# Optimization experiments

Hardware: AMD Instinct MI355X
Metric: run time of the kernel (lower is better)

## Reference

```python
import jax, jax.numpy as jnp
import numpy as np

EPS = 1e-5

def conv1x1(x, W, b):
    # x: (B,C,H,W), W: (O,C), b: (O,)
    return jnp.einsum('bchw,oc->bohw', x, W) + b[None, :, None, None]

def setup_inputs() -> dict:
    key = jax.random.key(0)
    ks = jax.random.split(key, 16)
    B, C_in, C1, D, K, H, Wd = 8, 512, 256, 128, 32, 96, 96
    s = lambda k, shape, fan: jax.random.normal(k, shape, jnp.float32) * (1.0 / np.sqrt(fan))
    return {
        'X': jax.random.normal(ks[0], (B, C_in, H, Wd), jnp.float32),
        'W_theta': s(ks[1], (C1, C_in), C_in), 'b_theta': jnp.zeros((C1,), jnp.float32),
        'W_phi': s(ks[2], (C1, C_in), C_in), 'b_phi': jnp.zeros((C1,), jnp.float32),
        'W_g': s(ks[3], (C1, C_in), C_in), 'b_g': jnp.zeros((C1,), jnp.float32),
        'W2': s(ks[4], (C_in, C1), C1), 'b2': jnp.zeros((C_in,), jnp.float32),
        'W3': s(ks[5], (D, C_in), C_in), 'b3': jnp.zeros((D,), jnp.float32),
        'codewords': jax.random.normal(ks[6], (K, D), jnp.float32),
        'scale': -jax.random.uniform(ks[7], (K,), jnp.float32),  # Deep-TEN init: U(-1,0)
        'W_fc': s(ks[8], (C_in, D), D), 'b_fc': jnp.zeros((C_in,), jnp.float32),
    }

def reference(X, W_theta, b_theta, W_phi, b_phi, W_g, b_g, W2, b2, W3, b3,
              codewords, scale, W_fc, b_fc):
    B, C_in, H, Wd = X.shape
    C1 = W_theta.shape[0]
    D, K = W3.shape[0], codewords.shape[0]
    N = H * Wd
    # --- non-local (channel-attention) block ---
    theta = conv1x1(X, W_theta, b_theta).reshape(B, C1, N)          # (B,C1,N)
    phi = conv1x1(X, W_phi, b_phi).reshape(B, C1, N)                # (B,C1,N)
    g = conv1x1(X, W_g, b_g).reshape(B, C1, N)                      # (B,C1,N)
    f = jax.nn.softmax(jnp.einsum('bcn,bdn->bcd', theta, phi), axis=-1)  # (B,C1,C1)
    y = jnp.einsum('bcd,bdn->bcn', f, g).reshape(B, C1, H, Wd)
    z = conv1x1(y, W2, b2) + X                                      # (B,C_in,H,W)
    # --- Deep-TEN encoding ---
    z_ = conv1x1(z, W3, b3)                                         # (B,D,H,W)
    x = z_.reshape(B, D, N).transpose(0, 2, 1)                      # (B,N,D)
    # squared L2 distances to codewords without (B,N,K,D) residuals
    dist = (jnp.sum(x * x, -1, keepdims=True)
            - 2.0 * jnp.einsum('bnd,kd->bnk', x, codewords)
            + jnp.sum(codewords * codewords, -1))                   # (B,N,K)
    A = jax.nn.softmax(scale * dist, axis=-1)                       # (B,N,K)
    # E_k = sum_i A_ik (x_i - c_k)
    E = jnp.einsum('bnk,bnd->bkd', A, x) - A.sum(1)[..., None] * codewords  # (B,K,D)
    # --- training-mode batch norm over K channels (no affine) ---
    mean = E.mean(axis=(0, 2), keepdims=True)
    var = E.var(axis=(0, 2), keepdims=True)
    e = jax.nn.relu((E - mean) * jax.lax.rsqrt(var + EPS))
    Es = e.sum(axis=1)                                              # (B,D)
    gamma = jax.nn.sigmoid(Es @ W_fc.T + b_fc)                      # (B,C_in)
    return z * gamma[:, :, None, None]
```

## Files before the change

### kernel.cpp

```cpp
#include <hip/hip_runtime.h>


typedef unsigned short u16;

#define Bb 8
#define Cc 512
#define C1 256
#define Dd 128
#define Kk 32
#define Nn 9216

typedef __attribute__((ext_vector_type(8))) short short8v;
typedef __attribute__((ext_vector_type(4))) short short4v;
typedef __attribute__((ext_vector_type(4))) float f32x4;

__device__ __forceinline__ float b2f(u16 u) {
  union { unsigned int i; float f; } v; v.i = ((unsigned int)u) << 16; return v.f;
}
__device__ __forceinline__ u16 f2b(float f) {
  union { float f; unsigned int i; } v; v.f = f;
  unsigned int x = v.i;
  return (u16)((x + 0x7fffu + ((x >> 16) & 1u)) >> 16);
}

__device__ __forceinline__ float4 load4(const float* p) { return *(const float4*)p; }
__device__ __forceinline__ float4 load4(const u16* p) {
  ushort4 q = *(const ushort4*)p;
  return make_float4(b2f(q.x), b2f(q.y), b2f(q.z), b2f(q.w));
}
__device__ __forceinline__ void store4(float* p, float a, float b, float c, float d) {
  *(float4*)p = make_float4(a, b, c, d);
}

__device__ __forceinline__ float waveSum(float v) {
  #pragma unroll
  for (int o = 32; o > 0; o >>= 1) v += __shfl_xor(v, o);
  return v;
}
__device__ __forceinline__ float waveMax(float v) {
  #pragma unroll
  for (int o = 32; o > 0; o >>= 1) v = fmaxf(v, __shfl_xor(v, o));
  return v;
}
__device__ __forceinline__ float blockSum256(float v) {
  __shared__ float sm[4];
  v = waveSum(v);
  if ((threadIdx.x & 63) == 0) sm[threadIdx.x >> 6] = v;
  __syncthreads();
  float r = sm[0] + sm[1] + sm[2] + sm[3];
  __syncthreads();
  return r;
}
__device__ __forceinline__ float blockMax256(float v) {
  __shared__ float sm[4];
  v = waveMax(v);
  if ((threadIdx.x & 63) == 0) sm[threadIdx.x >> 6] = v;
  __syncthreads();
  float r = fmaxf(fmaxf(sm[0], sm[1]), fmaxf(sm[2], sm[3]));
  __syncthreads();
  return r;
}

__device__ __forceinline__ f32x4 mfma_bf16_16x16x32(short8v a, short8v b, f32x4 c) {
  asm("v_mfma_f32_16x16x32_bf16 %0, %1, %2, %0" : "+v"(c) : "v"(a), "v"(b));
  return c;
}

__device__ __forceinline__ int fsw(int r) { return (r ^ (r >> 2) ^ (r >> 4)) & 3; }

__device__ __forceinline__ void cvt2(float x0, float x1, unsigned int& h, unsigned int& l) {
  asm("v_cvt_pk_bf16_f32 %0, %1, %2" : "=v"(h) : "v"(x0), "v"(x1));
  union { unsigned int u; float f; } fa, fb;
  fa.u = h << 16; fb.u = h & 0xffff0000u;
  float r0 = x0 - fa.f, r1 = x1 - fb.f;
  asm("v_cvt_pk_bf16_f32 %0, %1, %2" : "=v"(l) : "v"(r0), "v"(r1));
}

__device__ __forceinline__ void storeC4(float* p, float4 v) { *(float4*)p = v; }
__device__ __forceinline__ void storeC4(u16* p, float4 v) {
  ushort4 q; q.x = f2b(v.x); q.y = f2b(v.y); q.z = f2b(v.z); q.w = f2b(v.w);
  *(ushort4*)p = q;
}

template<typename TO, int OMODE, bool ADDI>
__global__ __launch_bounds__(256, 3) void gemm_mfma(
    const float* __restrict__ A, const float* __restrict__ B, TO* __restrict__ C,
    int N, int K,
    long long sA, long long sB, long long sC,
    const float* __restrict__ biasRow, long long sBias,
    int gnx, int gny)
{
  __shared__ __align__(16) u16 Asm_[2][128][40];
  __shared__ __align__(16) u16 Bsm_[2][128][40];

  int id = blockIdx.x;
  {
    const int nwg = gridDim.x;
    if ((nwg & 7) == 0) id = (id & 7) * (nwg >> 3) + (id >> 3);
  }
  const int per = gnx * gny;
  const int b = id / per;
  const int rem = id - b * per;
  const int by = rem % gny;
  const int bx = rem / gny;
  A += b * sA; B += b * sB; C += b * sC;
  const int m0 = by * 128, n0 = bx * 128;

  const int t = threadIdx.x;
  const int w = t >> 6, lane = t & 63;
  const int wr = w >> 1, wc = w & 1;
  const int lr = lane & 15, lq = lane >> 4;

  const int sar = t >> 1, sak = (t & 1) * 16;
  const int kg2 = t >> 4, ng = t & 15;

  float ra[16];
  float rb[16];

  auto loadA = [&](int k0) {
    const float* p = A + (long long)(m0 + sar) * K + (k0 + sak);
    #pragma unroll
    for (int i = 0; i < 4; ++i) {
      float4 v = *(const float4*)(p + i * 4);
      ra[i*4+0] = v.x; ra[i*4+1] = v.y; ra[i*4+2] = v.z; ra[i*4+3] = v.w;
    }
  };
  auto loadB = [&](int k0) {
    const float* p = B + (long long)(k0 + kg2 * 2) * N + (n0 + ng * 8);
    #pragma unroll
    for (int i = 0; i < 2; ++i) {
      float4 v0 = *(const float4*)(p + (long long)i * N);
      float4 v1 = *(const float4*)(p + (long long)i * N + 4);
      rb[i*8+0]=v0.x; rb[i*8+1]=v0.y; rb[i*8+2]=v0.z; rb[i*8+3]=v0.w;
      rb[i*8+4]=v1.x; rb[i*8+5]=v1.y; rb[i*8+6]=v1.z; rb[i*8+7]=v1.w;
    }
  };

  auto stage = [&]() {
    {
      const int f = fsw(sar);
      #pragma unroll
      for (int h = 0; h < 2; ++h) {
        const int col = ((((sak >> 3) + h) ^ f) << 3);
        union { unsigned int u[4]; short8v v; } H, L;
        #pragma unroll
        for (int p = 0; p < 4; ++p) cvt2(ra[h*8+2*p], ra[h*8+2*p+1], H.u[p], L.u[p]);
        *(short8v*)&Asm_[0][sar][col] = H.v;
        *(short8v*)&Asm_[1][sar][col] = L.v;
      }
    }
    {
      const int blk = kg2 >> 2, sub = 2 * (kg2 & 3);
      #pragma unroll
      for (int j = 0; j < 8; ++j) {
        const int n = ng * 8 + j;
        const int col = ((blk ^ fsw(n)) << 3) + sub;
        unsigned int H, L;
        cvt2(rb[j], rb[8 + j], H, L);
        *(unsigned int*)&Bsm_[0][n][col] = H;
        *(unsigned int*)&Bsm_[1][n][col] = L;
      }
    }
  };

  f32x4 acc[4][4];
  #pragma unroll
  for (int im = 0; im < 4; ++im)
    #pragma unroll
    for (int in = 0; in < 4; ++in)
      acc[im][in] = f32x4{0.f, 0.f, 0.f, 0.f};

  loadA(0); loadB(0);
  for (int k0 = 0; k0 < K; k0 += 32) {
    stage();
    if (k0 + 32 < K) { loadA(k0 + 32); loadB(k0 + 32); }
    __syncthreads();
    short8v af[2][4];
    #pragma unroll
    for (int im = 0; im < 4; ++im) {
      const int r = wr * 64 + im * 16 + lr;
      const int col = ((lq ^ fsw(r)) << 3);
      af[0][im] = *(const short8v*)&Asm_[0][r][col];
      af[1][im] = *(const short8v*)&Asm_[1][r][col];
    }
    #pragma unroll
    for (int in = 0; in < 4; ++in) {
      const int rB = wc * 64 + in * 16 + lr;
      const int colB = ((lq ^ fsw(rB)) << 3);
      short8v bh = *(const short8v*)&Bsm_[0][rB][colB];
      short8v bl = *(const short8v*)&Bsm_[1][rB][colB];
      #pragma unroll
      for (int im = 0; im < 4; ++im) {
        acc[im][in] = mfma_bf16_16x16x32(af[0][im], bh, acc[im][in]);
        acc[im][in] = mfma_bf16_16x16x32(af[0][im], bl, acc[im][in]);
        acc[im][in] = mfma_bf16_16x16x32(af[1][im], bh, acc[im][in]);
      }
    }
    __syncthreads();
  }
  asm volatile("s_nop 7\n\ts_nop 7\n\ts_nop 7");

  if constexpr (OMODE == 1) {
    const float* bb = biasRow + (long long)b * sBias;
    #pragma unroll
    for (int im = 0; im < 4; ++im) {
      #pragma unroll
      for (int in = 0; in < 4; ++in) {
        const f32x4 a = acc[im][in];
        const int gc = n0 + wc * 64 + in * 16 + lr;
        const int d0b = wr * 64 + im * 16 + lq * 4;
        float4 v = make_float4(a[0] + bb[d0b + 0], a[1] + bb[d0b + 1],
                               a[2] + bb[d0b + 2], a[3] + bb[d0b + 3]);
        storeC4(&C[(long long)gc * Dd + d0b], v);
      }
    }
  } else {
    #pragma unroll
    for (int im = 0; im < 4; ++im) {
      #pragma unroll
      for (int in = 0; in < 4; ++in) {
        const f32x4 a = acc[im][in];
        const int gc = n0 + wc * 64 + in * 16 + lr;
        #pragma unroll
        for (int p = 0; p < 4; ++p) {
          const int gr = m0 + wr * 64 + im * 16 + lq * 4 + p;
          float v = a[p];
          if (biasRow) v += biasRow[b * sBias + gr];
          if (ADDI && gr == gc) v += 1.f;
          C[(long long)gr * N + gc] = v;
        }
      }
    }
  }
}

__device__ __constant__ int PIa[10] = {0,0,0,0,1,1,1,2,2,3};
__device__ __constant__ int PJa[10] = {0,1,2,3,1,2,3,2,3,3};

__global__ __launch_bounds__(256, 3) void gxxt_kernel(
    const float* __restrict__ X, float* __restrict__ part,
    int numKS, int kChunk, float* __restrict__ sP)
{
  __shared__ __align__(16) u16 Asm_[2][128][40];
  __shared__ __align__(16) u16 Bsm_[2][64][40];

  int id = blockIdx.x;
  {
    const int nwg = gridDim.x;
    if ((nwg & 7) == 0) id = (id & 7) * (nwg >> 3) + (id >> 3);
  }
  const int sub = id % 20;
  const int pair = sub >> 1, jh = sub & 1;
  const int rest = id / 20;
  const int ks = rest % numKS;
  const int b = rest / numKS;
  const int i0 = PIa[pair] * 128, j0 = PJa[pair] * 128;
  const bool same = (i0 == j0);
  const bool doSum = same && (jh == 0);
  const float* Xb = X + (long long)b * Cc * Nn;
  const int kBeg = ks * kChunk, kEnd = kBeg + kChunk;

  const int t = threadIdx.x;
  const int w = t >> 6, lane = t & 63;
  const int wr = w >> 1, wc = w & 1;
  const int lr = lane & 15, lq = lane >> 4;
  const int sar = t >> 1, sak = (t & 1) * 16;
  const int sbr = t >> 2, sbk = (t & 3) * 8;

  float ra[16], rb[8];
  float rs = 0.f;

  auto loadA = [&](int k0) {
    const float* p = Xb + (long long)(i0 + sar) * Nn + (k0 + sak);
    #pragma unroll
    for (int i = 0; i < 4; ++i) {
      float4 v = *(const float4*)(p + i * 4);
      ra[i*4+0] = v.x; ra[i*4+1] = v.y; ra[i*4+2] = v.z; ra[i*4+3] = v.w;
    }
  };
  auto loadB = [&](int k0) {
    const float* p = Xb + (long long)(j0 + jh * 64 + sbr) * Nn + (k0 + sbk);
    float4 v0 = *(const float4*)(p);
    float4 v1 = *(const float4*)(p + 4);
    rb[0]=v0.x; rb[1]=v0.y; rb[2]=v0.z; rb[3]=v0.w;
    rb[4]=v1.x; rb[5]=v1.y; rb[6]=v1.z; rb[7]=v1.w;
  };
  auto stageA = [&]() {
    const int f = fsw(sar);
    #pragma unroll
    for (int h = 0; h < 2; ++h) {
      const int col = ((((sak >> 3) + h) ^ f) << 3);
      union { unsigned int u[4]; short8v v; } Hv, Lv;
      #pragma unroll
      for (int p = 0; p < 4; ++p) cvt2(ra[h*8+2*p], ra[h*8+2*p+1], Hv.u[p], Lv.u[p]);
      *(short8v*)&Asm_[0][sar][col] = Hv.v;
      *(short8v*)&Asm_[1][sar][col] = Lv.v;
    }
  };
  auto stageB = [&]() {
    const int col = (((sbk >> 3) ^ fsw(sbr)) << 3);
    union { unsigned int u[4]; short8v v; } Hv, Lv;
    #pragma unroll
    for (int p = 0; p < 4; ++p) cvt2(rb[2*p], rb[2*p+1], Hv.u[p], Lv.u[p]);
    *(short8v*)&Bsm_[0][sbr][col] = Hv.v;
    *(short8v*)&Bsm_[1][sbr][col] = Lv.v;
  };

  f32x4 acc[4][2];
  #pragma unroll
  for (int im = 0; im < 4; ++im)
    #pragma unroll
    for (int in = 0; in < 2; ++in)
      acc[im][in] = f32x4{0.f, 0.f, 0.f, 0.f};

  loadA(kBeg);
  if (!same) loadB(kBeg);
  for (int k0 = kBeg; k0 < kEnd; k0 += 32) {
    if (doSum) {
      #pragma unroll
      for (int j = 0; j < 16; ++j) rs += ra[j];
    }
    stageA();
    if (!same) stageB();
    if (k0 + 32 < kEnd) { loadA(k0 + 32); if (!same) loadB(k0 + 32); }
    __syncthreads();
    short8v af[2][4];
    #pragma unroll
    for (int im = 0; im < 4; ++im) {
      const int r = wr * 64 + im * 16 + lr;
      const int col = ((lq ^ fsw(r)) << 3);
      af[0][im] = *(const short8v*)&Asm_[0][r][col];
      af[1][im] = *(const short8v*)&Asm_[1][r][col];
    }
    #pragma unroll
    for (int in = 0; in < 2; ++in) {
      const int rloc = wc * 32 + in * 16 + lr;
      short8v bh, bl;
      if (same) {
        const int r = jh * 64 + rloc;
        const int colB = ((lq ^ fsw(r)) << 3);
        bh = *(const short8v*)&Asm_[0][r][colB];
        bl = *(const short8v*)&Asm_[1][r][colB];
      } else {
        const int colB = ((lq ^ fsw(rloc)) << 3);
        bh = *(const short8v*)&Bsm_[0][rloc][colB];
        bl = *(const short8v*)&Bsm_[1][rloc][colB];
      }
      #pragma unroll
      for (int im = 0; im < 4; ++im) {
        acc[im][in] = mfma_bf16_16x16x32(af[0][im], bh, acc[im][in]);
        acc[im][in] = mfma_bf16_16x16x32(af[0][im], bl, acc[im][in]);
        acc[im][in] = mfma_bf16_16x16x32(af[1][im], bh, acc[im][in]);
      }
    }
    __syncthreads();
  }
  asm volatile("s_nop 7\n\ts_nop 7\n\ts_nop 7");

  if (doSum) sP[((long long)ks * Bb + b) * Cc + i0 + sar] = rs;

  float* Cp = part + ((long long)(ks * Bb + b) * 10 + pair) * 16384 + jh * 64;
  #pragma unroll
  for (int im = 0; im < 4; ++im) {
    #pragma unroll
    for (int in = 0; in < 2; ++in) {
      const f32x4 a = acc[im][in];
      const int gc = wc * 32 + in * 16 + lr;
      #pragma unroll
      for (int p = 0; p < 4; ++p) {
        const int gr = wr * 64 + im * 16 + lq * 4 + p;
        Cp[gr * 128 + gc] = a[p];
      }
    }
  }
}

__global__ __launch_bounds__(256) void gred_kernel(const float* __restrict__ part,
    float* __restrict__ G, int numKS) {
  __shared__ float sm[64][129];
  const int pair = blockIdx.x % 10, b = blockIdx.x / 10;
  const int i0 = PIa[pair] * 128, j0 = PJa[pair] * 128;
  float* Gb = G + (long long)b * Cc * Cc;
  const long long ksStr = (long long)Bb * 10 * 16384;
  const float* p0 = part + ((long long)b * 10 + pair) * 16384;
  const int t = threadIdx.x;
  for (int half = 0; half < 2; ++half) {
    const int r0 = half * 64;
    __syncthreads();
    for (int rep = 0; rep < 32; ++rep) {
      int idx = r0 * 128 + rep * 256 + t;
      float s = 0.f;
      for (int ks = 0; ks < numKS; ++ks) s += p0[(long long)ks * ksStr + idx];
      int r = (idx >> 7) - r0, c = idx & 127;
      sm[r][c] = s;
      Gb[(long long)(i0 + r0 + r) * Cc + (j0 + c)] = s;
    }
    if (i0 != j0) {
      __syncthreads();
      for (int rep = 0; rep < 32; ++rep) {
        int o = rep * 256 + t;
        int rr = o >> 6, cc = o & 63;
        Gb[(long long)(j0 + rr) * Cc + (i0 + r0 + cc)] = sm[cc][rr];
      }
    }
  }
}

template<bool TRANSB>
__global__ __launch_bounds__(256) void gemm64(
    const float* __restrict__ A, const float* __restrict__ B, float* __restrict__ C,
    int M, int N, int K,
    long long sA, long long sB, long long sC,
    const float* __restrict__ biasRow, long long sBias)
{
  const int bz = blockIdx.z;
  A += (long long)bz * sA;
  B += (long long)bz * sB;
  C += (long long)bz * sC;
  const int m0 = blockIdx.y * 64, n0 = blockIdx.x * 64;
  __shared__ __align__(16) float As[16][64];
  __shared__ __align__(16) float Bs[16][64];
  const int t = threadIdx.x;
  const int lr = t >> 2, lk = (t & 3) << 2;
  const int tm = (t >> 4) << 2, tn = (t & 15) << 2;
  float acc[4][4] = {};
  for (int k0 = 0; k0 < K; k0 += 16) {
    {
      float4 a = load4(A + (long long)(m0 + lr) * K + (k0 + lk));
      As[lk + 0][lr] = a.x; As[lk + 1][lr] = a.y; As[lk + 2][lr] = a.z; As[lk + 3][lr] = a.w;
    }
    if (TRANSB) {
      float4 b = load4(B + (long long)(n0 + lr) * K + (k0 + lk));
      Bs[lk + 0][lr] = b.x; Bs[lk + 1][lr] = b.y; Bs[lk + 2][lr] = b.z; Bs[lk + 3][lr] = b.w;
    } else {
      const int kr = t >> 4, nc = (t & 15) << 2;
      float4 b = load4(B + (long long)(k0 + kr) * N + (n0 + nc));
      *(float4*)&Bs[kr][nc] = b;
    }
    __syncthreads();
    #pragma unroll
    for (int kk = 0; kk < 16; ++kk) {
      const float4 av = *(const float4*)&As[kk][tm];
      const float4 bv = *(const float4*)&Bs[kk][tn];
      acc[0][0] = fmaf(av.x, bv.x, acc[0][0]);
      acc[0][1] = fmaf(av.x, bv.y, acc[0][1]);
      acc[0][2] = fmaf(av.x, bv.z, acc[0][2]);
      acc[0][3] = fmaf(av.x, bv.w, acc[0][3]);
      acc[1][0] = fmaf(av.y, bv.x, acc[1][0]);
      acc[1][1] = fmaf(av.y, bv.y, acc[1][1]);
      acc[1][2] = fmaf(av.y, bv.z, acc[1][2]);
      acc[1][3] = fmaf(av.y, bv.w, acc[1][3]);
      acc[2][0] = fmaf(av.z, bv.x, acc[2][0]);
      acc[2][1] = fmaf(av.z, bv.y, acc[2][1]);
      acc[2][2] = fmaf(av.z, bv.z, acc[2][2]);
      acc[2][3] = fmaf(av.z, bv.w, acc[2][3]);
      acc[3][0] = fmaf(av.w, bv.x, acc[3][0]);
      acc[3][1] = fmaf(av.w, bv.y, acc[3][1]);
      acc[3][2] = fmaf(av.w, bv.z, acc[3][2]);
      acc[3][3] = fmaf(av.w, bv.w, acc[3][3]);
    }
    __syncthreads();
  }
  #pragma unroll
  for (int i = 0; i < 4; ++i) {
    const int m = m0 + tm + i;
    float bias = biasRow ? biasRow[bz * sBias + m] : 0.f;
    store4(C + (long long)m * N + (n0 + tn),
           acc[i][0] + bias, acc[i][1] + bias, acc[i][2] + bias, acc[i][3] + bias);
  }
}

__global__ __launch_bounds__(256) void gemv2_kernel(const float* __restrict__ Wth,
    const float* __restrict__ Wph, const float* __restrict__ sP, int numKS,
    float* __restrict__ u, float* __restrict__ v) {
  int b = blockIdx.x & 7, sel = blockIdx.x >> 3;
  const float* W = sel ? Wph : Wth;
  float* out = sel ? v : u;
  __shared__ float ssm[Cc];
  for (int i = threadIdx.x; i < Cc; i += 256) {
    float s = 0.f;
    for (int ks = 0; ks < numKS; ++ks) s += sP[((long long)ks * Bb + b) * Cc + i];
    ssm[i] = s;
  }
  __syncthreads();
  int i = threadIdx.x;
  const float* wr = W + i * Cc;
  float acc = 0.f;
  for (int k = 0; k < Cc; ++k) acc = fmaf(wr[k], ssm[k], acc);
  out[b * C1 + i] = acc;
}

__global__ __launch_bounds__(256) void softmax_kernel(float* __restrict__ L,
    const float* __restrict__ bth, const float* __restrict__ bph,
    const float* __restrict__ u, const float* __restrict__ v,
    const float* __restrict__ bg, float* __restrict__ w) {
  __shared__ float bgs[C1];
  int row = blockIdx.x;
  int b = row >> 8, i = row & 255;
  int j = threadIdx.x;
  bgs[j] = bg[j];
  float bt = bth[i], bp = bph[j];
  long long idx = (long long)row * C1 + j;
  float val = L[idx] + bt * v[b * C1 + j] + u[b * C1 + i] * bp + (float)Nn * bt * bp;
  float mx = blockMax256(val);
  float p = expf(val - mx);
  float sm = blockSum256(p);
  float f = p / sm;
  L[idx] = f;
  float ws = blockSum256(f * bgs[j]);
  if (j == 0) w[row] = ws;
}

__global__ __launch_bounds__(256) void q_kernel(const float* __restrict__ W2,
                                                const float* __restrict__ b2v,
                                                const float* __restrict__ w,
                                                float* __restrict__ q) {
  int gi = blockIdx.x * 256 + threadIdx.x;
  int b = gi >> 9, c = gi & 511;
  __shared__ float wsm[C1];
  wsm[threadIdx.x] = w[b * C1 + threadIdx.x];
  __syncthreads();
  const float* wr = W2 + c * C1;
  float acc = b2v[c];
  for (int i = 0; i < C1; ++i) acc = fmaf(wr[i], wsm[i], acc);
  q[gi] = acc;
}

__global__ __launch_bounds__(256) void zqbias_kernel(const float* __restrict__ W3,
    const float* __restrict__ b3, const float* __restrict__ q, float* __restrict__ zqb) {
  int gi = blockIdx.x * 256 + threadIdx.x;
  int b = gi >> 7, d = gi & 127;
  const float* wr = W3 + d * Cc;
  const float* qr = q + b * Cc;
  float acc = b3[d];
  for (int c = 0; c < Cc; ++c) acc = fmaf(wr[c], qr[c], acc);
  zqb[gi] = acc;
}

template<typename ZT>
__global__ __launch_bounds__(256) void enc_kernel(
    const ZT* __restrict__ zq,
    const float* __restrict__ cw,
    const float* __restrict__ sc,
    float* __restrict__ Eraw8,
    float* __restrict__ Asum8)
{
  __shared__ float csm[Kk][Dd + 1];
  __shared__ float cc[Kk], ssm[Kk];
  __shared__ float sA[Kk][256 + 1];
  __shared__ float zs[16][Dd + 4];
  const int tid = threadIdx.x;
  const int b = blockIdx.y;
  const int slot = blockIdx.x & 7;
  const int n0 = blockIdx.x * 256;

  #pragma unroll
  for (int r = 0; r < 16; ++r) {
    int idx = r * 256 + tid;
    csm[idx >> 7][idx & 127] = cw[idx];
  }
  if (tid < Kk) ssm[tid] = sc[tid];
  __syncthreads();
  if (tid < Kk) {
    float a = 0.f;
    for (int d = 0; d < Dd; ++d) { float cv = csm[tid][d]; a = fmaf(cv, cv, a); }
    cc[tid] = a;
  }
  __syncthreads();

  const ZT* zrow = zq + ((long long)b * Nn + n0 + tid) * Dd;
  float dots[Kk];
  #pragma unroll
  for (int k = 0; k < Kk; ++k) dots[k] = 0.f;
  float xx = 0.f;
  for (int d = 0; d < Dd; d += 4) {
    float4 xv = load4(zrow + d);
    xx = fmaf(xv.x, xv.x, xx); xx = fmaf(xv.y, xv.y, xx);
    xx = fmaf(xv.z, xv.z, xx); xx = fmaf(xv.w, xv.w, xx);
    #pragma unroll
    for (int k = 0; k < Kk; ++k) {
      float dk = dots[k];
      dk = fmaf(csm[k][d + 0], xv.x, dk);
      dk = fmaf(csm[k][d + 1], xv.y, dk);
      dk = fmaf(csm[k][d + 2], xv.z, dk);
      dk = fmaf(csm[k][d + 3], xv.w, dk);
      dots[k] = dk;
    }
  }
  float mx = -1e30f;
  #pragma unroll
  for (int k = 0; k < Kk; ++k) {
    float l = ssm[k] * (xx - 2.f * dots[k] + cc[k]);
    dots[k] = l;
    mx = fmaxf(mx, l);
  }
  float sum = 0.f;
  #pragma unroll
  for (int k = 0; k < Kk; ++k) { float p = expf(dots[k] - mx); dots[k] = p; sum += p; }
  float inv = 1.f / sum;
  #pragma unroll
  for (int k = 0; k < Kk; ++k) sA[k][tid] = dots[k] * inv;
  __syncthreads();
  if (tid < Kk) {
    float s = 0.f;
    for (int p = 0; p < 256; ++p) s += sA[tid][p];
    atomicAdd(&Asum8[((long long)slot * Bb + b) * Kk + tid], s);
  }

  float acc[16];
  #pragma unroll
  for (int j = 0; j < 16; ++j) acc[j] = 0.f;
  const int k = tid & 31, d0 = (tid >> 5) * 16;
  const int spx = tid >> 4, sd = (tid & 15) * 8;
  for (int it = 0; it < 16; ++it) {
    __syncthreads();
    {
      const ZT* src = zq + ((long long)b * Nn + n0 + it * 16 + spx) * Dd + sd;
      float4 a4 = load4(src);
      float4 b4 = load4(src + 4);
      *(float4*)&zs[spx][sd] = a4;
      *(float4*)&zs[spx][sd + 4] = b4;
    }
    __syncthreads();
    #pragma unroll
    for (int p = 0; p < 16; ++p) {
      float a = sA[k][it * 16 + p];
      #pragma unroll
      for (int j = 0; j < 16; ++j) acc[j] = fmaf(a, zs[p][d0 + j], acc[j]);
    }
  }
  float* Ep = Eraw8 + (((long long)slot * Bb + b) * Kk + k) * Dd + d0;
  #pragma unroll
  for (int j = 0; j < 16; ++j) atomicAdd(Ep + j, acc[j]);
}

__global__ __launch_bounds__(256) void bn_kernel(const float* __restrict__ Eraw8,
    const float* __restrict__ Asum8, const float* __restrict__ cw, float* __restrict__ Es) {
  __shared__ float sas[8];
  int k = blockIdx.x, tid = threadIdx.x;
  if (tid < 8) {
    float a = 0.f;
    for (int sl = 0; sl < 8; ++sl) a += Asum8[((long long)sl * Bb + tid) * Kk + k];
    sas[tid] = a;
  }
  __syncthreads();
  float vals[4], s = 0.f, s2 = 0.f;
  #pragma unroll
  for (int r = 0; r < 4; ++r) {
    int i = r * 256 + tid;
    int b = i >> 7, d = i & 127;
    float e = 0.f;
    for (int sl = 0; sl < 8; ++sl)
      e += Eraw8[(((long long)sl * Bb + b) * Kk + k) * Dd + d];
    e -= sas[b] * cw[k * Dd + d];
    vals[r] = e; s += e; s2 = fmaf(e, e, s2);
  }
  s = blockSum256(s);
  s2 = blockSum256(s2);
  float mean = s * (1.f / 1024.f);
  float var = fmaxf(s2 * (1.f / 1024.f) - mean * mean, 0.f);
  float rs = rsqrtf(var + 1e-5f);
  #pragma unroll
  for (int r = 0; r < 4; ++r) {
    int i = r * 256 + tid;
    int b = i >> 7, d = i & 127;
    float e = (vals[r] - mean) * rs;
    if (e > 0.f) atomicAdd(&Es[b * Dd + d], e);
  }
}

__global__ __launch_bounds__(256) void gamma_kernel(const float* __restrict__ Es,
    const float* __restrict__ Wfc, const float* __restrict__ bfc,
    float* __restrict__ gam, float* __restrict__ q) {
  int gi = blockIdx.x * 256 + threadIdx.x;
  int b = gi >> 9, c = gi & 511;
  __shared__ float esm[Dd];
  if (threadIdx.x < Dd) esm[threadIdx.x] = Es[b * Dd + threadIdx.x];
  __syncthreads();
  const float* wr = Wfc + c * Dd;
  float acc = bfc[c];
  for (int d = 0; d < Dd; ++d) acc = fmaf(wr[d], esm[d], acc);
  float g = 1.f / (1.f + expf(-acc));
  gam[gi] = g;
  q[gi] *= g;
}

__global__ __launch_bounds__(256) void scaleP_kernel(float* __restrict__ P,
    const float* __restrict__ gam) {
  long long f = ((long long)blockIdx.x * 256 + threadIdx.x) * 4;
  int b = (int)(f >> 18), c = (int)((f >> 9) & 511);
  float g = gam[b * Cc + c];
  float4 v = *(const float4*)(P + f);
  store4(P + f, v.x * g, v.y * g, v.z * g, v.w * g);
}

extern "C" void kernel_launch(void* const* d_in, const int* in_sizes, int n_in,
                              void* d_out, int out_size, void* d_ws, size_t ws_size,
                              hipStream_t stream) {
  const float* X   = (const float*)d_in[0];
  const float* Wth = (const float*)d_in[1];
  const float* bth = (const float*)d_in[2];
  const float* Wph = (const float*)d_in[3];
  const float* bph = (const float*)d_in[4];
  const float* Wg  = (const float*)d_in[5];
  const float* bg  = (const float*)d_in[6];
  const float* W2  = (const float*)d_in[7];
  const float* b2v = (const float*)d_in[8];
  const float* W3  = (const float*)d_in[9];
  const float* b3v = (const float*)d_in[10];
  const float* CW  = (const float*)d_in[11];
  const float* SC  = (const float*)d_in[12];
  const float* Wfc = (const float*)d_in[13];
  const float* bfc = (const float*)d_in[14];
  float* out = (float*)d_out;
  float* wsf = (float*)d_ws;

  const long long szL   = (long long)Bb * C1 * C1;
  const long long szRA  = (long long)Bb * Cc * Cc;
  const long long szRB  = (long long)Bb * C1 * Cc;
  long long off = 0;
  float* s_   = wsf + off; off += Bb * Cc;
  float* u_   = wsf + off; off += Bb * C1;
  float* v_   = wsf + off; off += Bb * C1;
  float* w_   = wsf + off; off += Bb * C1;
  float* q_   = wsf + off; off += Bb * Cc;
  float* sP_  = wsf + off; off += (long long)Bb * Kk * Dd;
  float* EsL_ = wsf + off; off += Bb * Dd;
  float* Asum_= wsf + off; off += Bb * Kk;
  float* gam_ = wsf + off; off += Bb * Cc;
  float* L_   = wsf + off; off += szL;
  float* regA = wsf + off; off += szRA;
  float* regB = wsf + off; off += szRB;
  const long long baseFloats = off;
  float* tail = wsf + off;
  const long long ZQ_F  = (long long)Bb * Dd * Nn;
  const long long tailFloats = (long long)(ws_size / 4) - baseFloats;
  const bool big = tailFloats >= ZQ_F;
  const int numKS = big ? 4 : 2;
  float* part = tail;
  float* zqf  = tail;
  u16*   zqh  = (u16*)tail;
  float* R_   = L_;
  float* zqb_ = u_;
  float* E8_  = regB;
  float* A8_  = regB + 262144;
  float* Es_  = regB + 264192;
  (void)s_; (void)Asum_; (void)EsL_;

  const long long strX = (long long)Cc * Nn;
  const long long sG = (long long)Cc * Cc;
  const long long sU = (long long)C1 * Cc;
  const long long sL = (long long)C1 * C1;
  const long long sR = (long long)Dd * Cc;

  gxxt_kernel<<<dim3(20 * numKS * Bb), 256, 0, stream>>>(X, part, numKS, Nn / numKS, sP_);
  gred_kernel<<<dim3(10 * Bb), 256, 0, stream>>>(part, regA, numKS);
  gemm_mfma<float, 0, false><<<dim3(64), 256, 0, stream>>>(
      Wth, regA, regB, Cc, Cc, 0, sG, sU, nullptr, 0, 4, 2);
  gemv2_kernel<<<16, 256, 0, stream>>>(Wth, Wph, sP_, numKS, u_, v_);
  gemm64<true><<<dim3(4, 4, Bb), 256, 0, stream>>>(
      regB, Wph, L_, C1, C1, Cc, sU, 0, sL, nullptr, 0);
  softmax_kernel<<<Bb * C1, 256, 0, stream>>>(L_, bth, bph, u_, v_, bg, w_);
  gemm_mfma<float, 0, false><<<dim3(64), 256, 0, stream>>>(
      L_, Wg, regB, Cc, C1, sL, 0, sU, nullptr, 0, 4, 2);
  q_kernel<<<16, 256, 0, stream>>>(W2, b2v, w_, q_);
  gemm_mfma<float, 0, true><<<dim3(128), 256, 0, stream>>>(
      W2, regB, regA, Cc, C1, 0, sU, sG, nullptr, 0, 4, 4);
  hipMemsetAsync(regB, 0, (size_t)(262144 + 2048 + 1024) * 4, stream);
  gemm_mfma<float, 0, false><<<dim3(32), 256, 0, stream>>>(
      W3, regA, R_, Cc, Cc, 0, sG, sR, nullptr, 0, 4, 1);
  zqbias_kernel<<<4, 256, 0, stream>>>(W3, b3v, q_, zqb_);
  if (big) {
    gemm_mfma<float, 1, false><<<dim3(576), 256, 0, stream>>>(
        R_, X, zqf, Nn, Cc, sR, strX, (long long)Dd * Nn, zqb_, Dd, 72, 1);
    enc_kernel<float><<<dim3(36, Bb), 256, 0, stream>>>(zqf, CW, SC, E8_, A8_);
  } else {
    gemm_mfma<u16, 1, false><<<dim3(576), 256, 0, stream>>>(
        R_, X, zqh, Nn, Cc, sR, strX, (long long)Dd * Nn, zqb_, Dd, 72, 1);
    enc_kernel<u16><<<dim3(36, Bb), 256, 0, stream>>>(zqh, CW, SC, E8_, A8_);
  }
  bn_kernel<<<Kk, 256, 0, stream>>>(E8_, A8_, CW, Es_);
  gamma_kernel<<<16, 256, 0, stream>>>(Es_, Wfc, bfc, gam_, q_);
  scaleP_kernel<<<2048, 256, 0, stream>>>(regA, gam_);
  gemm_mfma<float, 0, false><<<dim3(2304), 256, 0, stream>>>(
      regA, X, out, Nn, Cc, sG, strX, strX, q_, Cc, 72, 4);
  (void)in_sizes; (void)n_in; (void)out_size;
}
```

Baseline: 895.9 us.

## Use full 128x128 tiles in Gram kernel and raise K-split count

The X·X^T Gram kernel now computes each 128x128 upper-triangle tile in one workgroup instead of splitting it into two 64-column halves, so the A rows are loaded and converted once per tile instead of twice. Each wave now holds a 4x4 accumulator grid. To keep enough workgroups in flight, the K-split count in the big-workspace path goes from 4 to 6. This adds register pressure, a larger B shared buffer and more partial sums for the reduction kernel to combine.

After: 911.9 us. About the same (+1.8%).

```diff
diff --git a/kernel.cpp b/kernel.cpp
--- a/kernel.cpp
+++ b/kernel.cpp
@@ -242,21 +242,19 @@
     int numKS, int kChunk, float* __restrict__ sP)
 {
   __shared__ __align__(16) u16 Asm_[2][128][40];
-  __shared__ __align__(16) u16 Bsm_[2][64][40];
+  __shared__ __align__(16) u16 Bsm_[2][128][40];
 
   int id = blockIdx.x;
   {
     const int nwg = gridDim.x;
     if ((nwg & 7) == 0) id = (id & 7) * (nwg >> 3) + (id >> 3);
   }
-  const int sub = id % 20;
-  const int pair = sub >> 1, jh = sub & 1;
-  const int rest = id / 20;
+  const int pair = id % 10;
+  const int rest = id / 10;
   const int ks = rest % numKS;
   const int b = rest / numKS;
   const int i0 = PIa[pair] * 128, j0 = PJa[pair] * 128;
   const bool same = (i0 == j0);
-  const bool doSum = same && (jh == 0);
   const float* Xb = X + (long long)b * Cc * Nn;
   const int kBeg = ks * kChunk, kEnd = kBeg + kChunk;
 
@@ -265,9 +263,8 @@
   const int wr = w >> 1, wc = w & 1;
   const int lr = lane & 15, lq = lane >> 4;
   const int sar = t >> 1, sak = (t & 1) * 16;
-  const int sbr = t >> 2, sbk = (t & 3) * 8;
-
-  float ra[16], rb[8];
+
+  float ra[16], rb[16];
   float rs = 0.f;
 
   auto loadA = [&](int k0) {
@@ -279,49 +276,45 @@
     }
   };
   auto loadB = [&](int k0) {
-    const float* p = Xb + (long long)(j0 + jh * 64 + sbr) * Nn + (k0 + sbk);
-    float4 v0 = *(const float4*)(p);
-    float4 v1 = *(const float4*)(p + 4);
-    rb[0]=v0.x; rb[1]=v0.y; rb[2]=v0.z; rb[3]=v0.w;
-    rb[4]=v1.x; rb[5]=v1.y; rb[6]=v1.z; rb[7]=v1.w;
+    const float* p = Xb + (long long)(j0 + sar) * Nn + (k0 + sak);
+    #pragma unroll
+    for (int i = 0; i < 4; ++i) {
+      float4 v = *(const float4*)(p + i * 4);
+      rb[i*4+0] = v.x; rb[i*4+1] = v.y; rb[i*4+2] = v.z; rb[i*4+3] = v.w;
+    }
   };
-  auto stageA = [&]() {
+  auto stageRow = [&](const float* s16, u16 (*H)[40], u16 (*L)[40]) {
     const int f = fsw(sar);
     #pragma unroll
     for (int h = 0; h < 2; ++h) {
       const int col = ((((sak >> 3) + h) ^ f) << 3);
       union { unsigned int u[4]; short8v v; } Hv, Lv;
       #pragma unroll
-      for (int p = 0; p < 4; ++p) cvt2(ra[h*8+2*p], ra[h*8+2*p+1], Hv.u[p], Lv.u[p]);
-      *(short8v*)&Asm_[0][sar][col] = Hv.v;
-      *(short8v*)&Asm_[1][sar][col] = Lv.v;
+      for (int p = 0; p < 4; ++p) cvt2(s16[h*8+2*p], s16[h*8+2*p+1], Hv.u[p], Lv.u[p]);
+      *(short8v*)&H[sar][col] = Hv.v;
+      *(short8v*)&L[sar][col] = Lv.v;
     }
   };
-  auto stageB = [&]() {
-    const int col = (((sbk >> 3) ^ fsw(sbr)) << 3);
-    union { unsigned int u[4]; short8v v; } Hv, Lv;
-    #pragma unroll
-    for (int p = 0; p < 4; ++p) cvt2(rb[2*p], rb[2*p+1], Hv.u[p], Lv.u[p]);
-    *(short8v*)&Bsm_[0][sbr][col] = Hv.v;
-    *(short8v*)&Bsm_[1][sbr][col] = Lv.v;
-  };
-
-  f32x4 acc[4][2];
+
+  const u16 (*BH)[40] = same ? Asm_[0] : Bsm_[0];
+  const u16 (*BL)[40] = same ? Asm_[1] : Bsm_[1];
+
+  f32x4 acc[4][4];
   #pragma unroll
   for (int im = 0; im < 4; ++im)
     #pragma unroll
-    for (int in = 0; in < 2; ++in)
+    for (int in = 0; in < 4; ++in)
       acc[im][in] = f32x4{0.f, 0.f, 0.f, 0.f};
 
   loadA(kBeg);
   if (!same) loadB(kBeg);
   for (int k0 = kBeg; k0 < kEnd; k0 += 32) {
-    if (doSum) {
+    if (same) {
       #pragma unroll
       for (int j = 0; j < 16; ++j) rs += ra[j];
     }
-    stageA();
-    if (!same) stageB();
+    stageRow(ra, Asm_[0], Asm_[1]);
+    if (!same) stageRow(rb, Bsm_[0], Bsm_[1]);
     if (k0 + 32 < kEnd) { loadA(k0 + 32); if (!same) loadB(k0 + 32); }
     __syncthreads();
     short8v af[2][4];
@@ -333,19 +326,11 @@
       af[1][im] = *(const short8v*)&Asm_[1][r][col];
     }
     #pragma unroll
-    for (int in = 0; in < 2; ++in) {
-      const int rloc = wc * 32 + in * 16 + lr;
-      short8v bh, bl;
-      if (same) {
-        const int r = jh * 64 + rloc;
-        const int colB = ((lq ^ fsw(r)) << 3);
-        bh = *(const short8v*)&Asm_[0][r][colB];
-        bl = *(const short8v*)&Asm_[1][r][colB];
-      } else {
-        const int colB = ((lq ^ fsw(rloc)) << 3);
-        bh = *(const short8v*)&Bsm_[0][rloc][colB];
-        bl = *(const short8v*)&Bsm_[1][rloc][colB];
-      }
+    for (int in = 0; in < 4; ++in) {
+      const int rB = wc * 64 + in * 16 + lr;
+      const int colB = ((lq ^ fsw(rB)) << 3);
+      short8v bh = *(const short8v*)&BH[rB][colB];
+      short8v bl = *(const short8v*)&BL[rB][colB];
       #pragma unroll
       for (int im = 0; im < 4; ++im) {
         acc[im][in] = mfma_bf16_16x16x32(af[0][im], bh, acc[im][in]);
@@ -357,15 +342,15 @@
   }
   asm volatile("s_nop 7\n\ts_nop 7\n\ts_nop 7");
 
-  if (doSum) sP[((long long)ks * Bb + b) * Cc + i0 + sar] = rs;
-
-  float* Cp = part + ((long long)(ks * Bb + b) * 10 + pair) * 16384 + jh * 64;
+  if (same) sP[((long long)ks * Bb + b) * Cc + i0 + sar] = rs;
+
+  float* Cp = part + ((long long)(ks * Bb + b) * 10 + pair) * 16384;
   #pragma unroll
   for (int im = 0; im < 4; ++im) {
     #pragma unroll
-    for (int in = 0; in < 2; ++in) {
+    for (int in = 0; in < 4; ++in) {
       const f32x4 a = acc[im][in];
-      const int gc = wc * 32 + in * 16 + lr;
+      const int gc = wc * 64 + in * 16 + lr;
       #pragma unroll
       for (int p = 0; p < 4; ++p) {
         const int gr = wr * 64 + im * 16 + lq * 4 + p;
@@ -736,7 +721,7 @@
   const long long ZQ_F  = (long long)Bb * Dd * Nn;
   const long long tailFloats = (long long)(ws_size / 4) - baseFloats;
   const bool big = tailFloats >= ZQ_F;
-  const int numKS = big ? 4 : 2;
+  const int numKS = big ? 6 : 2;
   float* part = tail;
   float* zqf  = tail;
   u16*   zqh  = (u16*)tail;
@@ -753,7 +738,7 @@
   const long long sL = (long long)C1 * C1;
   const long long sR = (long long)Dd * Cc;
 
-  gxxt_kernel<<<dim3(20 * numKS * Bb), 256, 0, stream>>>(X, part, numKS, Nn / numKS, sP_);
+  gxxt_kernel<<<dim3(10 * numKS * Bb), 256, 0, stream>>>(X, part, numKS, Nn / numKS, sP_);
   gred_kernel<<<dim3(10 * Bb), 256, 0, stream>>>(part, regA, numKS);
   gemm_mfma<float, 0, false><<<dim3(64), 256, 0, stream>>>(
       Wth, regA, regB, Cc, Cc, 0, sG, sU, nullptr, 0, 4, 2);
```
